# Optimization experiments

Hardware: AMD Instinct MI355X
Metric: run time of the kernel (lower is better)

The kernel has to match this reference:

```python
import jax, jax.numpy as jnp
import numpy as np

NUM_ATOMS = 512
NUM_DIMS = 128
H = 32
W = 32
B = 32


def make_dct_dict():
    # rows i: cos((2n+1) * i * pi / (2*num_dims)), L2-normalized; Dict = weights.T -> [D, A]
    i = jnp.arange(NUM_ATOMS, dtype=jnp.float32)[:, None]
    n = jnp.arange(NUM_DIMS, dtype=jnp.float32)[None, :]
    atoms = jnp.cos((2.0 * n + 1.0) * i * (np.pi / (2.0 * NUM_DIMS)))  # [A, D]
    atoms = atoms / jnp.linalg.norm(atoms, axis=1, keepdims=True)
    return atoms.T  # [D, A]


def setup_inputs() -> dict:
    key = jax.random.key(0)
    x = jax.random.normal(key, (B, NUM_DIMS, H, W), dtype=jnp.float32)
    Dict = make_dct_dict()                      # [D, A] learned param (DCT init)
    L = jnp.sum(Dict ** 2)                      # ||Dict||_F^2 (scalar param)
    alpha = jnp.ones((1, H, W, 1), dtype=jnp.float32)  # learned threshold param
    return {"x": x, "Dict": Dict, "alpha": alpha, "L": L, "num_iters": 16}


def reference(x, Dict, alpha, L, num_iters):
    l = alpha / L                                # [1,H,W,1] threshold, broadcasts over atoms
    xt = jnp.transpose(x, (0, 2, 3, 1))          # [B,H,W,D]
    S = (jnp.eye(NUM_ATOMS, dtype=Dict.dtype) - (Dict.T @ Dict) / L).T  # [A,A]
    y = xt @ Dict                                # [B,H,W,A]

    def soft_thresh(v):
        return jnp.sign(v) * jnp.maximum(jnp.abs(v) - l, 0.0)

    z = soft_thresh(y)

    def body(z, _):
        z = soft_thresh(z @ S + y / L)
        return z, None

    z, _ = jax.lax.scan(body, z, None, length=num_iters)
    x_recon = z @ Dict.T                         # [B,H,W,D]
    return (jnp.transpose(z, (0, 3, 1, 2)),      # [B,A,H,W]
            jnp.transpose(x_recon, (0, 3, 1, 2)),  # [B,D,H,W]
            Dict)
```

## Files before the change

### kernel.cpp

```cpp
#include <hip/hip_runtime.h>
#include <hip/hip_bf16.h>

typedef __bf16 bf16_t;
typedef bf16_t bf16x8 __attribute__((ext_vector_type(8)));
typedef float f32x4 __attribute__((ext_vector_type(4)));
typedef unsigned short u16;
typedef unsigned int u32;

static __device__ __forceinline__ u16 f2bf(float f) {
    __hip_bfloat16 h = __float2bfloat16(f);
    return __builtin_bit_cast(u16, h);
}
static __device__ __forceinline__ bf16_t fb(float f) {
    return __builtin_bit_cast(bf16_t, f2bf(f));
}
static __device__ __forceinline__ float bf2f(u16 u) {
    u32 x = ((u32)u) << 16;
    return __builtin_bit_cast(float, x);
}
static __device__ __forceinline__ float softthr(float v, float l) {
    return copysignf(fmaxf(fabsf(v) - l, 0.0f), v);
}

__global__ __launch_bounds__(256) void copy_dict(const float* __restrict__ Dict,
                                                 float* __restrict__ outd)
{
    int i = blockIdx.x * 256 + threadIdx.x;
    outd[i] = Dict[i];
}

__global__ __launch_bounds__(512, 2)
void lista_main(const float* __restrict__ x,
                const float* __restrict__ Dict,
                const float* __restrict__ alpha,
                const float* __restrict__ Lp,
                const int* __restrict__ nip,
                float* __restrict__ outz,
                float* __restrict__ outr)
{
    __shared__ __align__(16) u16 zl[32 * 512];
    __shared__ __align__(16) u16 rl[32 * 128];

    const int t = threadIdx.x;
    const int lane = t & 63;
    const int l15 = lane & 15;
    const int lg = lane >> 4;
    const int wave = t >> 6;
    const int bb = blockIdx.x >> 5;
    const int hw0 = (blockIdx.x & 31) << 5;
    const float invL = 1.0f / Lp[0];
    const int niter = nip[0];

    const int dimb = wave << 4;
    const int atb  = wave << 6;

    for (int i = t; i < 32 * 128; i += 512) {
        int d = i >> 5, px = i & 31;
        float v = x[((bb * 128 + d) << 10) + hw0 + px];
        rl[((px << 7) + d) ^ ((px & 7) << 3)] = f2bf(v);
    }

    float xpk[2][4];
#pragma unroll
    for (int nt = 0; nt < 2; ++nt)
#pragma unroll
        for (int rr = 0; rr < 4; ++rr)
            xpk[nt][rr] = x[((bb * 128 + dimb + lg * 4 + rr) << 10) + hw0 + nt * 16 + l15];

    float thr[2];
#pragma unroll
    for (int nt = 0; nt < 2; ++nt)
        thr[nt] = alpha[hw0 + nt * 16 + l15] * invL;

    bf16x8 g1a[16];
    {
        const float* drow = Dict + ((dimb + l15) << 9);
#pragma unroll
        for (int kt = 0; kt < 16; ++kt) {
            f32x4 c0 = *reinterpret_cast<const f32x4*>(&drow[kt * 32 + lg * 8]);
            f32x4 c1 = *reinterpret_cast<const f32x4*>(&drow[kt * 32 + lg * 8 + 4]);
#pragma unroll
            for (int j = 0; j < 4; ++j) {
                g1a[kt][j] = fb(-c0[j]);
                g1a[kt][j + 4] = fb(-c1[j]);
            }
        }
    }
    bf16x8 g2a[4][4];
#pragma unroll
    for (int at = 0; at < 4; ++at)
#pragma unroll
        for (int kt = 0; kt < 4; ++kt)
#pragma unroll
            for (int j = 0; j < 8; ++j)
                g2a[at][kt][j] = fb(Dict[((kt * 32 + lg * 8 + j) << 9) + atb + at * 16 + l15]);

    __syncthreads();

    auto run_g1 = [&](f32x4 (&a1)[2]) {
#pragma unroll
        for (int nt = 0; nt < 2; ++nt) {
            a1[nt][0] = xpk[nt][0];
            a1[nt][1] = xpk[nt][1];
            a1[nt][2] = xpk[nt][2];
            a1[nt][3] = xpk[nt][3];
        }
#pragma unroll
        for (int kt = 0; kt < 16; ++kt) {
            bf16x8 Bf[2];
#pragma unroll
            for (int nt = 0; nt < 2; ++nt) {
                int px = nt * 16 + l15;
                Bf[nt] = *reinterpret_cast<const bf16x8*>(
                    &zl[((px << 9) + kt * 32 + lg * 8) ^ ((px & 7) << 3)]);
            }
#pragma unroll
            for (int nt = 0; nt < 2; ++nt)
                a1[nt] = __builtin_amdgcn_mfma_f32_16x16x32_bf16(g1a[kt], Bf[nt], a1[nt], 0, 0, 0);
        }
    };

    f32x4 accz[4][2];
#pragma unroll
    for (int at = 0; at < 4; ++at)
#pragma unroll
        for (int nt = 0; nt < 2; ++nt)
            accz[at][nt] = f32x4{0.f, 0.f, 0.f, 0.f};

    for (int it = 0; it <= niter; ++it) {
        if (it > 0) {
            f32x4 a1[2];
            run_g1(a1);
#pragma unroll
            for (int nt = 0; nt < 2; ++nt) {
                int px = nt * 16 + l15;
                uint2 pk;
                pk.x = (u32)f2bf(a1[nt][0] * invL) | ((u32)f2bf(a1[nt][1] * invL) << 16);
                pk.y = (u32)f2bf(a1[nt][2] * invL) | ((u32)f2bf(a1[nt][3] * invL) << 16);
                *reinterpret_cast<uint2*>(
                    &rl[((px << 7) + dimb + lg * 4) ^ ((px & 7) << 3)]) = pk;
            }
            __syncthreads();
        }

#pragma unroll
        for (int kt = 0; kt < 4; ++kt) {
            bf16x8 Bf[2];
#pragma unroll
            for (int nt = 0; nt < 2; ++nt) {
                int px = nt * 16 + l15;
                Bf[nt] = *reinterpret_cast<const bf16x8*>(
                    &rl[((px << 7) + kt * 32 + lg * 8) ^ ((px & 7) << 3)]);
            }
            __builtin_amdgcn_s_setprio(1);
#pragma unroll
            for (int at = 0; at < 4; ++at)
#pragma unroll
                for (int nt = 0; nt < 2; ++nt)
                    accz[at][nt] = __builtin_amdgcn_mfma_f32_16x16x32_bf16(
                        g2a[at][kt], Bf[nt], accz[at][nt], 0, 0, 0);
            __builtin_amdgcn_s_setprio(0);
        }

#pragma unroll
        for (int at = 0; at < 4; ++at)
#pragma unroll
            for (int nt = 0; nt < 2; ++nt) {
                int px = nt * 16 + l15;
                f32x4 a = accz[at][nt];
                a[0] = softthr(a[0], thr[nt]);
                a[1] = softthr(a[1], thr[nt]);
                a[2] = softthr(a[2], thr[nt]);
                a[3] = softthr(a[3], thr[nt]);
                accz[at][nt] = a;
                uint2 pk;
                pk.x = (u32)f2bf(a[0]) | ((u32)f2bf(a[1]) << 16);
                pk.y = (u32)f2bf(a[2]) | ((u32)f2bf(a[3]) << 16);
                *reinterpret_cast<uint2*>(
                    &zl[((px << 9) + atb + at * 16 + lg * 4) ^ ((px & 7) << 3)]) = pk;
            }
        __syncthreads();
    }

    f32x4 a1[2];
    run_g1(a1);

    for (int i = t; i < 32 * 512; i += 512) {
        int a = i >> 5, px = i & 31;
        float zv = bf2f(zl[((px << 9) + a) ^ ((px & 7) << 3)]);
        __builtin_nontemporal_store(zv, &outz[((bb * 512 + a) << 10) + hw0 + px]);
    }
    __syncthreads();

    float* wf = reinterpret_cast<float*>(zl);
#pragma unroll
    for (int nt = 0; nt < 2; ++nt) {
        int px = nt * 16 + l15;
#pragma unroll
        for (int rr = 0; rr < 4; ++rr)
            wf[((px << 7) + dimb + lg * 4 + rr) ^ ((px & 7) << 2)] = xpk[nt][rr] - a1[nt][rr];
    }
    __syncthreads();

    for (int i = t; i < 32 * 128; i += 512) {
        int d = i >> 5, px = i & 31;
        __builtin_nontemporal_store(wf[((px << 7) + d) ^ ((px & 7) << 2)],
                                    &outr[((bb * 128 + d) << 10) + hw0 + px]);
    }
}

extern "C" void kernel_launch(void* const* d_in, const int* in_sizes, int n_in,
                              void* d_out, int out_size, void* d_ws, size_t ws_size,
                              hipStream_t stream)
{
    const float* x     = (const float*)d_in[0];
    const float* Dict  = (const float*)d_in[1];
    const float* alpha = (const float*)d_in[2];
    const float* Lp    = (const float*)d_in[3];
    const int*   nip   = (const int*)d_in[4];

    float* outz = (float*)d_out;
    float* outr = outz + 32 * 512 * 1024;
    float* outd = outr + 32 * 128 * 1024;

    copy_dict<<<dim3(256), dim3(256), 0, stream>>>(Dict, outd);
    lista_main<<<dim3(1024), dim3(512), 0, stream>>>(x, Dict, alpha, Lp, nip,
                                                     outz, outr);
}
```

Before: 207.2 us.

## Split-K the z·Dictᵀ GEMM across waves with an LDS partial-sum reduction

The residual GEMM z@Dictᵀ used to be split by output dimension: each wave ran a serial 16-step K=512 MFMA chain with only two accumulators. It is now split-K over four atom groups, so each wave computes a 64-dim by 128-atom partial with eight independent accumulators. The partials are written as bf16 to a new LDS buffer, and a separate pass sums them with a bf16 copy of x to form the residual. This shortens the MFMA dependency chain and raises instruction-level parallelism. In exchange it adds LDS traffic, one more barrier per iteration and more shared memory, and rounding the partials to bf16 before summing adds precision error, including in the reconstruction output.

```diff
diff --git a/kernel.cpp b/kernel.cpp
--- a/kernel.cpp
+++ b/kernel.cpp
@@ -40,49 +40,48 @@
 {
     __shared__ __align__(16) u16 zl[32 * 512];
     __shared__ __align__(16) u16 rl[32 * 128];
+    __shared__ __align__(16) u16 xs[32 * 128];
+    __shared__ __align__(16) u16 pb[32 * 4 * 128];
 
     const int t = threadIdx.x;
     const int lane = t & 63;
     const int l15 = lane & 15;
     const int lg = lane >> 4;
     const int wave = t >> 6;
+    const int dg = wave >> 2;
+    const int ag = wave & 3;
+    const int atb = wave << 6;
     const int bb = blockIdx.x >> 5;
     const int hw0 = (blockIdx.x & 31) << 5;
     const float invL = 1.0f / Lp[0];
     const int niter = nip[0];
 
-    const int dimb = wave << 4;
-    const int atb  = wave << 6;
+    const int rpx = t & 31;
+    const int roc = t >> 5;
 
     for (int i = t; i < 32 * 128; i += 512) {
         int d = i >> 5, px = i & 31;
-        float v = x[((bb * 128 + d) << 10) + hw0 + px];
-        rl[((px << 7) + d) ^ ((px & 7) << 3)] = f2bf(v);
-    }
-
-    float xpk[2][4];
-#pragma unroll
-    for (int nt = 0; nt < 2; ++nt)
-#pragma unroll
-        for (int rr = 0; rr < 4; ++rr)
-            xpk[nt][rr] = x[((bb * 128 + dimb + lg * 4 + rr) << 10) + hw0 + nt * 16 + l15];
+        xs[((px << 7) + d) ^ ((px & 7) << 3)] =
+            f2bf(x[((bb * 128 + d) << 10) + hw0 + px]);
+    }
 
     float thr[2];
 #pragma unroll
     for (int nt = 0; nt < 2; ++nt)
         thr[nt] = alpha[hw0 + nt * 16 + l15] * invL;
 
-    bf16x8 g1a[16];
-    {
-        const float* drow = Dict + ((dimb + l15) << 9);
-#pragma unroll
-        for (int kt = 0; kt < 16; ++kt) {
-            f32x4 c0 = *reinterpret_cast<const f32x4*>(&drow[kt * 32 + lg * 8]);
-            f32x4 c1 = *reinterpret_cast<const f32x4*>(&drow[kt * 32 + lg * 8 + 4]);
+    bf16x8 g1a[4][4];
+#pragma unroll
+    for (int mt = 0; mt < 4; ++mt) {
+        const float* drow = Dict + ((dg * 64 + mt * 16 + l15) << 9) + ag * 128 + lg * 8;
+#pragma unroll
+        for (int kt = 0; kt < 4; ++kt) {
+            f32x4 c0 = *reinterpret_cast<const f32x4*>(drow + kt * 32);
+            f32x4 c1 = *reinterpret_cast<const f32x4*>(drow + kt * 32 + 4);
 #pragma unroll
             for (int j = 0; j < 4; ++j) {
-                g1a[kt][j] = fb(-c0[j]);
-                g1a[kt][j + 4] = fb(-c1[j]);
+                g1a[mt][kt][j] = fb(-c0[j]);
+                g1a[mt][kt][j + 4] = fb(-c1[j]);
             }
         }
     }
@@ -97,29 +96,6 @@
 
     __syncthreads();
 
-    auto run_g1 = [&](f32x4 (&a1)[2]) {
-#pragma unroll
-        for (int nt = 0; nt < 2; ++nt) {
-            a1[nt][0] = xpk[nt][0];
-            a1[nt][1] = xpk[nt][1];
-            a1[nt][2] = xpk[nt][2];
-            a1[nt][3] = xpk[nt][3];
-        }
-#pragma unroll
-        for (int kt = 0; kt < 16; ++kt) {
-            bf16x8 Bf[2];
-#pragma unroll
-            for (int nt = 0; nt < 2; ++nt) {
-                int px = nt * 16 + l15;
-                Bf[nt] = *reinterpret_cast<const bf16x8*>(
-                    &zl[((px << 9) + kt * 32 + lg * 8) ^ ((px & 7) << 3)]);
-            }
-#pragma unroll
-            for (int nt = 0; nt < 2; ++nt)
-                a1[nt] = __builtin_amdgcn_mfma_f32_16x16x32_bf16(g1a[kt], Bf[nt], a1[nt], 0, 0, 0);
-        }
-    };
-
     f32x4 accz[4][2];
 #pragma unroll
     for (int at = 0; at < 4; ++at)
@@ -127,22 +103,7 @@
         for (int nt = 0; nt < 2; ++nt)
             accz[at][nt] = f32x4{0.f, 0.f, 0.f, 0.f};
 
-    for (int it = 0; it <= niter; ++it) {
-        if (it > 0) {
-            f32x4 a1[2];
-            run_g1(a1);
-#pragma unroll
-            for (int nt = 0; nt < 2; ++nt) {
-                int px = nt * 16 + l15;
-                uint2 pk;
-                pk.x = (u32)f2bf(a1[nt][0] * invL) | ((u32)f2bf(a1[nt][1] * invL) << 16);
-                pk.y = (u32)f2bf(a1[nt][2] * invL) | ((u32)f2bf(a1[nt][3] * invL) << 16);
-                *reinterpret_cast<uint2*>(
-                    &rl[((px << 7) + dimb + lg * 4) ^ ((px & 7) << 3)]) = pk;
-            }
-            __syncthreads();
-        }
-
+    auto run_g2 = [&](const u16* __restrict__ bsrc) {
 #pragma unroll
         for (int kt = 0; kt < 4; ++kt) {
             bf16x8 Bf[2];
@@ -150,7 +111,7 @@
             for (int nt = 0; nt < 2; ++nt) {
                 int px = nt * 16 + l15;
                 Bf[nt] = *reinterpret_cast<const bf16x8*>(
-                    &rl[((px << 7) + kt * 32 + lg * 8) ^ ((px & 7) << 3)]);
+                    &bsrc[((px << 7) + kt * 32 + lg * 8) ^ ((px & 7) << 3)]);
             }
             __builtin_amdgcn_s_setprio(1);
 #pragma unroll
@@ -161,7 +122,6 @@
                         g2a[at][kt], Bf[nt], accz[at][nt], 0, 0, 0);
             __builtin_amdgcn_s_setprio(0);
         }
-
 #pragma unroll
         for (int at = 0; at < 4; ++at)
 #pragma unroll
@@ -179,11 +139,87 @@
                 *reinterpret_cast<uint2*>(
                     &zl[((px << 9) + atb + at * 16 + lg * 4) ^ ((px & 7) << 3)]) = pk;
             }
+    };
+
+    auto run_g1 = [&]() {
+        f32x4 a1p[4][2];
+#pragma unroll
+        for (int mt = 0; mt < 4; ++mt)
+#pragma unroll
+            for (int nt = 0; nt < 2; ++nt)
+                a1p[mt][nt] = f32x4{0.f, 0.f, 0.f, 0.f};
+#pragma unroll
+        for (int kt = 0; kt < 4; ++kt) {
+            bf16x8 Bf[2];
+#pragma unroll
+            for (int nt = 0; nt < 2; ++nt) {
+                int px = nt * 16 + l15;
+                Bf[nt] = *reinterpret_cast<const bf16x8*>(
+                    &zl[((px << 9) + ag * 128 + kt * 32 + lg * 8) ^ ((px & 7) << 3)]);
+            }
+            __builtin_amdgcn_s_setprio(1);
+#pragma unroll
+            for (int mt = 0; mt < 4; ++mt)
+#pragma unroll
+                for (int nt = 0; nt < 2; ++nt)
+                    a1p[mt][nt] = __builtin_amdgcn_mfma_f32_16x16x32_bf16(
+                        g1a[mt][kt], Bf[nt], a1p[mt][nt], 0, 0, 0);
+            __builtin_amdgcn_s_setprio(0);
+        }
+#pragma unroll
+        for (int mt = 0; mt < 4; ++mt)
+#pragma unroll
+            for (int nt = 0; nt < 2; ++nt) {
+                int px = nt * 16 + l15;
+                int d0 = dg * 64 + mt * 16 + lg * 4;
+                f32x4 a = a1p[mt][nt];
+                uint2 pk;
+                pk.x = (u32)f2bf(a[0]) | ((u32)f2bf(a[1]) << 16);
+                pk.y = (u32)f2bf(a[2]) | ((u32)f2bf(a[3]) << 16);
+                *reinterpret_cast<uint2*>(
+                    &pb[((px << 9) + (ag << 7) + d0) ^ ((px & 7) << 3)]) = pk;
+            }
+    };
+
+    run_g2(xs);
+    __syncthreads();
+
+    for (int it = 1; it <= niter; ++it) {
+        run_g1();
         __syncthreads();
-    }
-
-    f32x4 a1[2];
-    run_g1(a1);
+        {
+            const int sw = (rpx & 7) << 3;
+            bf16x8 p0 = *reinterpret_cast<const bf16x8*>(&pb[((rpx << 9) + 0 * 128 + roc * 8) ^ sw]);
+            bf16x8 p1 = *reinterpret_cast<const bf16x8*>(&pb[((rpx << 9) + 1 * 128 + roc * 8) ^ sw]);
+            bf16x8 p2 = *reinterpret_cast<const bf16x8*>(&pb[((rpx << 9) + 2 * 128 + roc * 8) ^ sw]);
+            bf16x8 p3 = *reinterpret_cast<const bf16x8*>(&pb[((rpx << 9) + 3 * 128 + roc * 8) ^ sw]);
+            bf16x8 xv = *reinterpret_cast<const bf16x8*>(&xs[((rpx << 7) + roc * 8) ^ sw]);
+            bf16x8 rv;
+#pragma unroll
+            for (int e = 0; e < 8; ++e) {
+                float s = ((float)xv[e] + (float)p0[e]) + ((float)p1[e] + (float)p2[e]) + (float)p3[e];
+                rv[e] = fb(s * invL);
+            }
+            *reinterpret_cast<bf16x8*>(&rl[((rpx << 7) + roc * 8) ^ sw]) = rv;
+        }
+        __syncthreads();
+        run_g2(rl);
+        __syncthreads();
+    }
+
+    run_g1();
+    __syncthreads();
+    float rec[8];
+    {
+        const int sw = (rpx & 7) << 3;
+        bf16x8 p0 = *reinterpret_cast<const bf16x8*>(&pb[((rpx << 9) + 0 * 128 + roc * 8) ^ sw]);
+        bf16x8 p1 = *reinterpret_cast<const bf16x8*>(&pb[((rpx << 9) + 1 * 128 + roc * 8) ^ sw]);
+        bf16x8 p2 = *reinterpret_cast<const bf16x8*>(&pb[((rpx << 9) + 2 * 128 + roc * 8) ^ sw]);
+        bf16x8 p3 = *reinterpret_cast<const bf16x8*>(&pb[((rpx << 9) + 3 * 128 + roc * 8) ^ sw]);
+#pragma unroll
+        for (int e = 0; e < 8; ++e)
+            rec[e] = -(((float)p0[e] + (float)p1[e]) + ((float)p2[e] + (float)p3[e]));
+    }
 
     for (int i = t; i < 32 * 512; i += 512) {
         int a = i >> 5, px = i & 31;
@@ -192,20 +228,23 @@
     }
     __syncthreads();
 
-    float* wf = reinterpret_cast<float*>(zl);
-#pragma unroll
-    for (int nt = 0; nt < 2; ++nt) {
-        int px = nt * 16 + l15;
-#pragma unroll
-        for (int rr = 0; rr < 4; ++rr)
-            wf[((px << 7) + dimb + lg * 4 + rr) ^ ((px & 7) << 2)] = xpk[nt][rr] - a1[nt][rr];
-    }
-    __syncthreads();
-
-    for (int i = t; i < 32 * 128; i += 512) {
-        int d = i >> 5, px = i & 31;
-        __builtin_nontemporal_store(wf[((px << 7) + d) ^ ((px & 7) << 2)],
-                                    &outr[((bb * 128 + d) << 10) + hw0 + px]);
+    {
+        float* wf = reinterpret_cast<float*>(pb);
+        const int swf = (rpx & 7) << 2;
+        f32x4 lo{rec[0], rec[1], rec[2], rec[3]};
+        f32x4 hi{rec[4], rec[5], rec[6], rec[7]};
+        *reinterpret_cast<f32x4*>(&wf[((rpx << 7) + roc * 8) ^ swf]) = lo;
+        *reinterpret_cast<f32x4*>(&wf[((rpx << 7) + roc * 8 + 4) ^ swf]) = hi;
+    }
+    __syncthreads();
+
+    {
+        const float* wf = reinterpret_cast<const float*>(pb);
+        for (int i = t; i < 32 * 128; i += 512) {
+            int d = i >> 5, px = i & 31;
+            __builtin_nontemporal_store(wf[((px << 7) + d) ^ ((px & 7) << 2)],
+                                        &outr[((bb * 128 + d) << 10) + hw0 + px]);
+        }
     }
 }
 
```

New measurement: 213.6 us. 1.03x slower.
